# Kernel tuning notes

Measured on AMD Instinct MI355X. Metric: run time of the kernel, lower is better.

Reference implementation:

```python
import jax, jax.numpy as jnp
import numpy as np

B, L, D_IN, D_OUT = 8, 2048, 256, 256


def setup_inputs() -> dict:
    key = jax.random.key(0)
    ks = jax.random.split(key, 7)
    s_in = 1.0 / np.sqrt(D_IN)
    return {
        "x": jax.random.normal(ks[0], (B, L, D_IN), dtype=jnp.float32),
        "Wq": jax.random.uniform(ks[1], (D_OUT, D_IN), jnp.float32, -s_in, s_in),
        "bq": jax.random.uniform(ks[2], (D_OUT,), jnp.float32, -s_in, s_in),
        "Wk": jax.random.uniform(ks[3], (D_OUT, D_IN), jnp.float32, -s_in, s_in),
        "bk": jax.random.uniform(ks[4], (D_OUT,), jnp.float32, -s_in, s_in),
        "Wv": jax.random.uniform(ks[5], (D_OUT, D_IN), jnp.float32, -s_in, s_in),
        "bv": jax.random.uniform(ks[6], (D_OUT,), jnp.float32, -s_in, s_in),
    }


def reference(x, Wq, bq, Wk, bk, Wv, bv):
    # QKV projections (torch Linear: y = x @ W.T + b)
    Q = jnp.einsum("bld,od->blo", x, Wq) + bq  # [B, L, D_OUT]
    K = jnp.einsum("bld,od->blo", x, Wk) + bk
    V = jnp.einsum("bld,od->blo", x, Wv) + bv
    scale = jnp.float32(D_OUT) ** 0.5
    E = jnp.einsum("bqd,bkd->bqk", Q, K) / scale  # [B, L, L]
    # NON-STANDARD: softmax over dim=1 (the query axis / columns of E)
    A = jax.nn.softmax(E, axis=1)
    C = jnp.einsum("bqk,bkd->bqd", A, V)  # [B, L, D_OUT]
    S_p = jnp.concatenate([Q, C], axis=1)  # [B, 2L, D_OUT]
    return (S_p, A)
```

## Files before the change

### kernel.cpp

```cpp
#include <hip/hip_runtime.h>
#include <hip/hip_bf16.h>
#include <stdint.h>

#define B_ 8
#define L_ 2048
#define D_ 256

typedef unsigned short u16;
typedef __attribute__((ext_vector_type(4))) float f32x4;
typedef __attribute__((ext_vector_type(8))) short bf16x8;
typedef __attribute__((ext_vector_type(4))) short s16x4;

__device__ __forceinline__ u16 f2b(float f) {
  union { float f; unsigned u; } v; v.f = f;
  unsigned r = v.u + 0x7FFFu + ((v.u >> 16) & 1u);
  return (u16)(r >> 16);
}

__device__ __forceinline__ float b2f(u16 h) {
  union { unsigned u; float f; } v; v.u = (unsigned)h << 16; return v.f;
}

__device__ __forceinline__ void comb(float& m, float& s, float m2, float s2) {
  float mn = fmaxf(m, m2);
  s = s * __expf(m - mn) + s2 * __expf(m2 - mn);
  m = mn;
}

__device__ __forceinline__ void async_copy16(const void* g, u16* l) {
  __builtin_amdgcn_global_load_lds(
      (const __attribute__((address_space(1))) unsigned*)g,
      (__attribute__((address_space(3))) unsigned*)l,
      16, 0, 0);
}

template<int KD>
__device__ __forceinline__ void gemm_core(const u16* __restrict__ Ag,
                                          const u16* __restrict__ Bg,
                                          int tile_m, int tile_n,
                                          u16* lds_a, u16* lds_b,
                                          f32x4 acc[4][4]) {
  const int tid  = threadIdx.x;
  const int wave = tid >> 6, lane = tid & 63;
  const int qd = lane >> 4, ln = lane & 15;
  const int wm = wave >> 1, wn = wave & 1;
  const int lrow = lane >> 2;
  const int lcol = (lane & 3) * 8;
  const u16* Abase = Ag + (size_t)tile_m * KD + lcol;
  const u16* Bbase = Bg + (size_t)tile_n * KD + lcol;

  for (int k0 = 0; k0 < KD; k0 += 32) {
#pragma unroll
    for (int j = 0; j < 2; ++j) {
      const int r0 = j * 64 + wave * 16;
      async_copy16(Abase + (size_t)(r0 + lrow) * KD + k0, lds_a + r0 * 32);
      async_copy16(Bbase + (size_t)(r0 + lrow) * KD + k0, lds_b + r0 * 32);
    }
    __syncthreads();
    bf16x8 af[4], bg[4];
#pragma unroll
    for (int i = 0; i < 4; ++i) {
      af[i] = *(const bf16x8*)(lds_a + (wm * 64 + i * 16 + ln) * 32 + qd * 8);
      bg[i] = *(const bf16x8*)(lds_b + (wn * 64 + i * 16 + ln) * 32 + qd * 8);
    }
#pragma unroll
    for (int i = 0; i < 4; ++i)
#pragma unroll
      for (int j = 0; j < 4; ++j)
        acc[i][j] = __builtin_amdgcn_mfma_f32_16x16x32_bf16(af[i], bg[j], acc[i][j], 0, 0, 0);
    __syncthreads();
  }
}

__global__ __launch_bounds__(256) void cvt_kernel(const float* __restrict__ x,
    const float* __restrict__ Wq, const float* __restrict__ Wk, const float* __restrict__ Wv,
    u16* __restrict__ xb, u16* __restrict__ Wb) {
  const int i = blockIdx.x * 256 + threadIdx.x;
  const int NX4 = (B_ * L_ * D_) / 4;
  f32x4 v;
  u16* dst;
  if (i < NX4) {
    v = ((const f32x4*)x)[i];
    dst = xb + (size_t)i * 4;
  } else {
    int wi = i - NX4;
    int z = wi >> 14;
    int off = wi & 16383;
    const float* W = (z == 0) ? Wq : (z == 1 ? Wk : Wv);
    v = ((const f32x4*)W)[off];
    dst = Wb + (size_t)z * 65536 + (size_t)off * 4;
  }
  unsigned p0 = (unsigned)f2b(v.x) | ((unsigned)f2b(v.y) << 16);
  unsigned p1 = (unsigned)f2b(v.z) | ((unsigned)f2b(v.w) << 16);
  *(uint2*)dst = make_uint2(p0, p1);
}

__global__ __launch_bounds__(256) void qkv_gemm(const u16* __restrict__ xb, const u16* __restrict__ Wb,
    const float* __restrict__ bq, const float* __restrict__ bk, const float* __restrict__ bv,
    u16* __restrict__ Qb, u16* __restrict__ Kb, u16* __restrict__ Vb,
    float* __restrict__ out_sp) {
  __shared__ u16 lds_a[128 * 32], lds_b[128 * 32];
  const int z = blockIdx.z;
  const float* bias = (z == 0) ? bq : (z == 1 ? bk : bv);
  u16* dst = (z == 0) ? Qb : (z == 1 ? Kb : Vb);
  const int tile_m = blockIdx.x * 128, tile_n = blockIdx.y * 128;
  f32x4 acc[4][4];
#pragma unroll
  for (int i = 0; i < 4; ++i)
#pragma unroll
    for (int j = 0; j < 4; ++j) acc[i][j] = (f32x4){0.f, 0.f, 0.f, 0.f};
  gemm_core<256>(xb, Wb + (size_t)z * 256 * 256, tile_m, tile_n, lds_a, lds_b, acc);

  const int lane = threadIdx.x & 63, wave = threadIdx.x >> 6;
  const int qd = lane >> 4, ln = lane & 15, wm = wave >> 1, wn = wave & 1;
#pragma unroll
  for (int i = 0; i < 4; ++i)
#pragma unroll
    for (int j = 0; j < 4; ++j) {
      const int col = tile_n + wn * 64 + j * 16 + ln;
      const float bvv = bias[col];
      const int row0 = tile_m + wm * 64 + i * 16 + qd * 4;
#pragma unroll
      for (int r = 0; r < 4; ++r) {
        const int row = row0 + r;
        const float val = acc[i][j][r] + bvv;
        dst[(size_t)row * D_ + col] = f2b(val);
        if (z == 0) {
          const int bb = row >> 11, l = row & 2047;
          out_sp[((size_t)bb * (2 * L_) + l) * D_ + col] = val;
        }
      }
    }
}

__global__ __launch_bounds__(256) void transpose_v(const u16* __restrict__ Vb, u16* __restrict__ Vbt) {
  const int b = blockIdx.z;
  const int l0 = blockIdx.x * 64;
  const int d0 = blockIdx.y * 64;
  __shared__ u16 t[64][65];
  const int tx = threadIdx.x & 63;
  const int ty = threadIdx.x >> 6;
  const u16* src = Vb + (size_t)b * L_ * D_;
  for (int j = ty; j < 64; j += 4)
    t[j][tx] = src[(size_t)(l0 + j) * D_ + d0 + tx];
  __syncthreads();
  u16* dst = Vbt + (size_t)b * D_ * L_;
  for (int j = ty; j < 64; j += 4)
    dst[(size_t)(d0 + j) * L_ + l0 + tx] = t[tx][j];
}

__global__ __launch_bounds__(256) void e_gemm(const u16* __restrict__ Qb, const u16* __restrict__ Kb,
                                              u16* __restrict__ Eb16,
                                              float* __restrict__ pm, float* __restrict__ ps) {
  __shared__ u16 lds_a[128 * 32], lds_b[128 * 32];
  __shared__ float sm_m[4][64], sm_s[4][64];
  const int b = blockIdx.z;
  const int tile_m = blockIdx.x * 128, tile_n = blockIdx.y * 128;
  f32x4 acc[4][4];
#pragma unroll
  for (int i = 0; i < 4; ++i)
#pragma unroll
    for (int j = 0; j < 4; ++j) acc[i][j] = (f32x4){0.f, 0.f, 0.f, 0.f};
  gemm_core<256>(Qb + (size_t)b * L_ * D_, Kb + (size_t)b * L_ * D_, tile_m, tile_n, lds_a, lds_b, acc);

  u16* Eb = Eb16 + (size_t)b * L_ * L_;
  const int tid = threadIdx.x;
  const int lane = tid & 63, wave = tid >> 6;
  const int qd = lane >> 4, ln = lane & 15, wm = wave >> 1, wn = wave & 1;
#pragma unroll
  for (int j = 0; j < 4; ++j) {
    const int col = tile_n + wn * 64 + j * 16 + ln;
    const int row0 = tile_m + wm * 64 + qd * 4;
    float m = -1e30f;
#pragma unroll
    for (int i = 0; i < 4; ++i)
#pragma unroll
      for (int r = 0; r < 4; ++r)
        m = fmaxf(m, acc[i][j][r] * 0.0625f);
    float s = 0.f;
#pragma unroll
    for (int i = 0; i < 4; ++i)
#pragma unroll
      for (int r = 0; r < 4; ++r) {
        const float e = acc[i][j][r] * 0.0625f;
        Eb[(size_t)(row0 + i * 16 + r) * L_ + col] = f2b(e);
        s += __expf(e - m);
      }
    comb(m, s, __shfl_xor(m, 16), __shfl_xor(s, 16));
    comb(m, s, __shfl_xor(m, 32), __shfl_xor(s, 32));
    if (qd == 0) { sm_m[wave][j * 16 + ln] = m; sm_s[wave][j * 16 + ln] = s; }
  }
  __syncthreads();
  if (tid < 128) {
    const int w = tid >> 6, c = tid & 63;
    float m = sm_m[w][c], s = sm_s[w][c];
    comb(m, s, sm_m[w + 2][c], sm_s[w + 2][c]);
    const size_t idx = (size_t)blockIdx.x * (B_ * L_) + (size_t)b * L_ + tile_n + w * 64 + c;
    pm[idx] = m;
    ps[idx] = s;
  }
}

__global__ __launch_bounds__(256) void stats_reduce(const float* __restrict__ pm,
                                                    const float* __restrict__ ps,
                                                    float* __restrict__ mOut, float* __restrict__ rOut) {
  const int idx = blockIdx.x * 256 + threadIdx.x;
  float m = -1e30f, s = 0.f;
#pragma unroll
  for (int t = 0; t < 16; ++t)
    comb(m, s, pm[t * (B_ * L_) + idx], ps[t * (B_ * L_) + idx]);
  mOut[idx] = m;
  rOut[idx] = 1.0f / s;
}

__global__ __launch_bounds__(256) void av_fused(const u16* __restrict__ Eb16, const u16* __restrict__ Vbt,
                                                const float* __restrict__ mArr, const float* __restrict__ rArr,
                                                float* __restrict__ Aout, float* __restrict__ out_sp) {
  __shared__ u16 lds_b[256 * 32];
  __shared__ u16 lds_a[32 * 32];
  const int b = blockIdx.y;
  const int tile_m = blockIdx.x * 32;
  const int tid = threadIdx.x;
  const int wave = tid >> 6, lane = tid & 63;
  const int qd = lane >> 4, ln = lane & 15;
  const int lrow = lane >> 2, lcol = (lane & 3) * 8;

  const u16* Vb_ = Vbt + (size_t)b * D_ * L_ + lcol;
  const int arow = tid >> 3, koff = (tid & 7) * 4;
  const u16* Erow = Eb16 + ((size_t)b * L_ + tile_m + arow) * L_ + koff;
  float* Arow = Aout + ((size_t)(b * L_ + tile_m + arow)) * L_ + koff;
  const float* mrow = mArr + (size_t)b * L_ + koff;
  const float* rrow = rArr + (size_t)b * L_ + koff;

  f32x4 acc[2][4];
#pragma unroll
  for (int i = 0; i < 2; ++i)
#pragma unroll
    for (int j = 0; j < 4; ++j) acc[i][j] = (f32x4){0.f, 0.f, 0.f, 0.f};

  for (int k0 = 0; k0 < L_; k0 += 32) {
#pragma unroll
    for (int jj = 0; jj < 4; ++jj) {
      const int r0 = wave * 64 + jj * 16;
      async_copy16(Vb_ + (size_t)(r0 + lrow) * L_ + k0, lds_b + r0 * 32);
    }
    s16x4 ev = *(const s16x4*)(Erow + k0);
    const f32x4 mv = *(const f32x4*)(mrow + k0);
    const f32x4 rv = *(const f32x4*)(rrow + k0);
    f32x4 a;
    a.x = __expf(b2f((u16)ev.x) - mv.x) * rv.x;
    a.y = __expf(b2f((u16)ev.y) - mv.y) * rv.y;
    a.z = __expf(b2f((u16)ev.z) - mv.z) * rv.z;
    a.w = __expf(b2f((u16)ev.w) - mv.w) * rv.w;
    *(f32x4*)(Arow + k0) = a;
    uint2 pk;
    pk.x = (unsigned)f2b(a.x) | ((unsigned)f2b(a.y) << 16);
    pk.y = (unsigned)f2b(a.z) | ((unsigned)f2b(a.w) << 16);
    *(uint2*)(lds_a + (size_t)tid * 4) = pk;
    __syncthreads();

    bf16x8 af[2], bg[4];
#pragma unroll
    for (int i = 0; i < 2; ++i)
      af[i] = *(const bf16x8*)(lds_a + (i * 16 + ln) * 32 + qd * 8);
#pragma unroll
    for (int j = 0; j < 4; ++j)
      bg[j] = *(const bf16x8*)(lds_b + (wave * 64 + j * 16 + ln) * 32 + qd * 8);
#pragma unroll
    for (int i = 0; i < 2; ++i)
#pragma unroll
      for (int j = 0; j < 4; ++j)
        acc[i][j] = __builtin_amdgcn_mfma_f32_16x16x32_bf16(af[i], bg[j], acc[i][j], 0, 0, 0);
    __syncthreads();
  }

#pragma unroll
  for (int i = 0; i < 2; ++i)
#pragma unroll
    for (int j = 0; j < 4; ++j) {
      const int col = wave * 64 + j * 16 + ln;
      const int row0 = tile_m + i * 16 + qd * 4;
#pragma unroll
      for (int r = 0; r < 4; ++r)
        out_sp[((size_t)b * (2 * L_) + L_ + row0 + r) * D_ + col] = acc[i][j][r];
    }
}

extern "C" void kernel_launch(void* const* d_in, const int* in_sizes, int n_in,
                              void* d_out, int out_size, void* d_ws, size_t ws_size,
                              hipStream_t stream) {
  const float* x  = (const float*)d_in[0];
  const float* Wq = (const float*)d_in[1];
  const float* bq = (const float*)d_in[2];
  const float* Wk = (const float*)d_in[3];
  const float* bk = (const float*)d_in[4];
  const float* Wv = (const float*)d_in[5];
  const float* bv = (const float*)d_in[6];

  float* out    = (float*)d_out;
  float* outA   = out + (size_t)B_ * (2 * L_) * D_;

  u16* w    = (u16*)d_ws;
  u16* xb   = w;
  u16* Wb   = xb + 4194304;
  u16* Qb   = Wb + 196608;
  u16* Kb   = Qb + 4194304;
  u16* Vb   = Kb + 4194304;
  u16* Vbt  = Vb + 4194304;
  u16* Eb16 = Vbt + 4194304;
  float* mArr = (float*)(Eb16 + 33554432);
  float* rArr = mArr + B_ * L_;
  float* pm   = rArr + B_ * L_;
  float* ps   = pm + 16 * B_ * L_;

  cvt_kernel<<<4288, 256, 0, stream>>>(x, Wq, Wk, Wv, xb, Wb);
  qkv_gemm<<<dim3(128, 2, 3), 256, 0, stream>>>(xb, Wb, bq, bk, bv, Qb, Kb, Vb, out);
  transpose_v<<<dim3(32, 4, 8), 256, 0, stream>>>(Vb, Vbt);
  e_gemm<<<dim3(16, 16, 8), 256, 0, stream>>>(Qb, Kb, Eb16, pm, ps);
  stats_reduce<<<64, 256, 0, stream>>>(pm, ps, mArr, rArr);
  av_fused<<<dim3(64, 8), 256, 0, stream>>>(Eb16, Vbt, mArr, rArr, outA, out);
}
```

Measured before the change: 319.1 us.

## Stage GEMM epilogues through LDS, fuse V transpose, widen AV k-step

The QKV and E GEMM epilogues now stage their bf16 results in shared memory and write them out as coalesced 16-byte rows instead of scattered 2-byte stores. The V projection writes its transposed layout directly, which removes the separate transpose kernel and its extra round trip through global memory. The av_fused loop now processes 64 columns per step with 8-wide loads and prefetches the next E, m and r values, halving the number of barriers. The cost is more shared-memory use in av_fused and extra barriers in the epilogues.

```diff
diff --git a/kernel.cpp b/kernel.cpp
--- a/kernel.cpp
+++ b/kernel.cpp
@@ -9,7 +9,6 @@
 typedef unsigned short u16;
 typedef __attribute__((ext_vector_type(4))) float f32x4;
 typedef __attribute__((ext_vector_type(8))) short bf16x8;
-typedef __attribute__((ext_vector_type(4))) short s16x4;
 
 __device__ __forceinline__ u16 f2b(float f) {
   union { float f; unsigned u; } v; v.f = f;
@@ -97,62 +96,92 @@
 
 __global__ __launch_bounds__(256) void qkv_gemm(const u16* __restrict__ xb, const u16* __restrict__ Wb,
     const float* __restrict__ bq, const float* __restrict__ bk, const float* __restrict__ bv,
-    u16* __restrict__ Qb, u16* __restrict__ Kb, u16* __restrict__ Vb,
+    u16* __restrict__ Qb, u16* __restrict__ Kb, u16* __restrict__ Vbt,
     float* __restrict__ out_sp) {
-  __shared__ u16 lds_a[128 * 32], lds_b[128 * 32];
+  __shared__ u16 lds[8192];
   const int z = blockIdx.z;
   const float* bias = (z == 0) ? bq : (z == 1 ? bk : bv);
-  u16* dst = (z == 0) ? Qb : (z == 1 ? Kb : Vb);
   const int tile_m = blockIdx.x * 128, tile_n = blockIdx.y * 128;
   f32x4 acc[4][4];
 #pragma unroll
   for (int i = 0; i < 4; ++i)
 #pragma unroll
     for (int j = 0; j < 4; ++j) acc[i][j] = (f32x4){0.f, 0.f, 0.f, 0.f};
-  gemm_core<256>(xb, Wb + (size_t)z * 256 * 256, tile_m, tile_n, lds_a, lds_b, acc);
-
-  const int lane = threadIdx.x & 63, wave = threadIdx.x >> 6;
+  gemm_core<256>(xb, Wb + (size_t)z * 256 * 256, tile_m, tile_n, lds, lds + 4096, acc);
+
+  const int tid = threadIdx.x, lane = tid & 63, wave = tid >> 6;
   const int qd = lane >> 4, ln = lane & 15, wm = wave >> 1, wn = wave & 1;
-#pragma unroll
-  for (int i = 0; i < 4; ++i)
-#pragma unroll
-    for (int j = 0; j < 4; ++j) {
-      const int col = tile_n + wn * 64 + j * 16 + ln;
-      const float bvv = bias[col];
-      const int row0 = tile_m + wm * 64 + i * 16 + qd * 4;
-#pragma unroll
-      for (int r = 0; r < 4; ++r) {
-        const int row = row0 + r;
-        const float val = acc[i][j][r] + bvv;
-        dst[(size_t)row * D_ + col] = f2b(val);
-        if (z == 0) {
-          const int bb = row >> 11, l = row & 2047;
-          out_sp[((size_t)bb * (2 * L_) + l) * D_ + col] = val;
-        }
+
+  if (z < 2) {
+    u16* dst = (z == 0) ? Qb : Kb;
+#pragma unroll
+    for (int p = 0; p < 2; ++p) {
+      __syncthreads();
+      if (wm == p) {
+#pragma unroll
+        for (int i = 0; i < 4; ++i)
+#pragma unroll
+          for (int j = 0; j < 4; ++j) {
+            const int col = wn * 64 + j * 16 + ln;
+            const float bvv = bias[tile_n + col];
+#pragma unroll
+            for (int r = 0; r < 4; ++r) {
+              const int row = i * 16 + qd * 4 + r;
+              const float val = acc[i][j][r] + bvv;
+              lds[row * 128 + col] = f2b(val);
+              if (z == 0) {
+                const int grow = tile_m + p * 64 + row;
+                const int bb = grow >> 11, l = grow & 2047;
+                out_sp[((size_t)bb * (2 * L_) + l) * D_ + tile_n + col] = val;
+              }
+            }
+          }
       }
-    }
-}
-
-__global__ __launch_bounds__(256) void transpose_v(const u16* __restrict__ Vb, u16* __restrict__ Vbt) {
-  const int b = blockIdx.z;
-  const int l0 = blockIdx.x * 64;
-  const int d0 = blockIdx.y * 64;
-  __shared__ u16 t[64][65];
-  const int tx = threadIdx.x & 63;
-  const int ty = threadIdx.x >> 6;
-  const u16* src = Vb + (size_t)b * L_ * D_;
-  for (int j = ty; j < 64; j += 4)
-    t[j][tx] = src[(size_t)(l0 + j) * D_ + d0 + tx];
-  __syncthreads();
-  u16* dst = Vbt + (size_t)b * D_ * L_;
-  for (int j = ty; j < 64; j += 4)
-    dst[(size_t)(d0 + j) * L_ + l0 + tx] = t[tx][j];
+      __syncthreads();
+      const int r = tid >> 2;
+#pragma unroll
+      for (int s = 0; s < 4; ++s) {
+        const int chunk = (tid & 3) + s * 4;
+        bf16x8 v = *(const bf16x8*)(lds + r * 128 + chunk * 8);
+        *(bf16x8*)(dst + (size_t)(tile_m + p * 64 + r) * D_ + tile_n + chunk * 8) = v;
+      }
+    }
+  } else {
+    const int bb = tile_m >> 11, l0 = tile_m & 2047;
+    u16* dstb = Vbt + (size_t)bb * D_ * L_;
+#pragma unroll
+    for (int p = 0; p < 2; ++p) {
+      __syncthreads();
+      if (wn == p) {
+#pragma unroll
+        for (int i = 0; i < 4; ++i)
+#pragma unroll
+          for (int j = 0; j < 4; ++j) {
+            const int col = j * 16 + ln;
+            const float bvv = bias[tile_n + p * 64 + col];
+#pragma unroll
+            for (int r = 0; r < 4; ++r) {
+              const int row = wm * 64 + i * 16 + qd * 4 + r;
+              lds[col * 128 + row] = f2b(acc[i][j][r] + bvv);
+            }
+          }
+      }
+      __syncthreads();
+      const int dr = tid >> 2;
+#pragma unroll
+      for (int s = 0; s < 4; ++s) {
+        const int chunk = (tid & 3) + s * 4;
+        bf16x8 v = *(const bf16x8*)(lds + dr * 128 + chunk * 8);
+        *(bf16x8*)(dstb + (size_t)(tile_n + p * 64 + dr) * L_ + l0 + chunk * 8) = v;
+      }
+    }
+  }
 }
 
 __global__ __launch_bounds__(256) void e_gemm(const u16* __restrict__ Qb, const u16* __restrict__ Kb,
                                               u16* __restrict__ Eb16,
                                               float* __restrict__ pm, float* __restrict__ ps) {
-  __shared__ u16 lds_a[128 * 32], lds_b[128 * 32];
+  __shared__ u16 lds[8192];
   __shared__ float sm_m[4][64], sm_s[4][64];
   const int b = blockIdx.z;
   const int tile_m = blockIdx.x * 128, tile_n = blockIdx.y * 128;
@@ -161,16 +190,15 @@
   for (int i = 0; i < 4; ++i)
 #pragma unroll
     for (int j = 0; j < 4; ++j) acc[i][j] = (f32x4){0.f, 0.f, 0.f, 0.f};
-  gemm_core<256>(Qb + (size_t)b * L_ * D_, Kb + (size_t)b * L_ * D_, tile_m, tile_n, lds_a, lds_b, acc);
+  gemm_core<256>(Qb + (size_t)b * L_ * D_, Kb + (size_t)b * L_ * D_, tile_m, tile_n, lds, lds + 4096, acc);
 
   u16* Eb = Eb16 + (size_t)b * L_ * L_;
   const int tid = threadIdx.x;
   const int lane = tid & 63, wave = tid >> 6;
   const int qd = lane >> 4, ln = lane & 15, wm = wave >> 1, wn = wave & 1;
+
 #pragma unroll
   for (int j = 0; j < 4; ++j) {
-    const int col = tile_n + wn * 64 + j * 16 + ln;
-    const int row0 = tile_m + wm * 64 + qd * 4;
     float m = -1e30f;
 #pragma unroll
     for (int i = 0; i < 4; ++i)
@@ -181,11 +209,8 @@
 #pragma unroll
     for (int i = 0; i < 4; ++i)
 #pragma unroll
-      for (int r = 0; r < 4; ++r) {
-        const float e = acc[i][j][r] * 0.0625f;
-        Eb[(size_t)(row0 + i * 16 + r) * L_ + col] = f2b(e);
-        s += __expf(e - m);
-      }
+      for (int r = 0; r < 4; ++r)
+        s += __expf(acc[i][j][r] * 0.0625f - m);
     comb(m, s, __shfl_xor(m, 16), __shfl_xor(s, 16));
     comb(m, s, __shfl_xor(m, 32), __shfl_xor(s, 32));
     if (qd == 0) { sm_m[wave][j * 16 + ln] = m; sm_s[wave][j * 16 + ln] = s; }
@@ -199,6 +224,32 @@
     pm[idx] = m;
     ps[idx] = s;
   }
+
+#pragma unroll
+  for (int p = 0; p < 2; ++p) {
+    __syncthreads();
+    if (wm == p) {
+#pragma unroll
+      for (int i = 0; i < 4; ++i)
+#pragma unroll
+        for (int j = 0; j < 4; ++j) {
+          const int col = wn * 64 + j * 16 + ln;
+#pragma unroll
+          for (int r = 0; r < 4; ++r) {
+            const int row = i * 16 + qd * 4 + r;
+            lds[row * 128 + col] = f2b(acc[i][j][r] * 0.0625f);
+          }
+        }
+    }
+    __syncthreads();
+    const int r = tid >> 2;
+#pragma unroll
+    for (int s = 0; s < 4; ++s) {
+      const int chunk = (tid & 3) + s * 4;
+      bf16x8 v = *(const bf16x8*)(lds + r * 128 + chunk * 8);
+      *(bf16x8*)(Eb + (size_t)(tile_m + p * 64 + r) * L_ + tile_n + chunk * 8) = v;
+    }
+  }
 }
 
 __global__ __launch_bounds__(256) void stats_reduce(const float* __restrict__ pm,
@@ -216,19 +267,19 @@
 __global__ __launch_bounds__(256) void av_fused(const u16* __restrict__ Eb16, const u16* __restrict__ Vbt,
                                                 const float* __restrict__ mArr, const float* __restrict__ rArr,
                                                 float* __restrict__ Aout, float* __restrict__ out_sp) {
-  __shared__ u16 lds_b[256 * 32];
-  __shared__ u16 lds_a[32 * 32];
+  __shared__ u16 lds_b[256 * 64];
+  __shared__ u16 lds_a[32 * 64];
   const int b = blockIdx.y;
   const int tile_m = blockIdx.x * 32;
   const int tid = threadIdx.x;
   const int wave = tid >> 6, lane = tid & 63;
   const int qd = lane >> 4, ln = lane & 15;
-  const int lrow = lane >> 2, lcol = (lane & 3) * 8;
+  const int lrow = lane >> 3, lcol = (lane & 7) * 8;
 
   const u16* Vb_ = Vbt + (size_t)b * D_ * L_ + lcol;
-  const int arow = tid >> 3, koff = (tid & 7) * 4;
+  const int arow = tid >> 3, koff = (tid & 7) * 8;
   const u16* Erow = Eb16 + ((size_t)b * L_ + tile_m + arow) * L_ + koff;
-  float* Arow = Aout + ((size_t)(b * L_ + tile_m + arow)) * L_ + koff;
+  float* Arow = Aout + ((size_t)b * L_ + tile_m + arow) * L_ + koff;
   const float* mrow = mArr + (size_t)b * L_ + koff;
   const float* rrow = rArr + (size_t)b * L_ + koff;
 
@@ -238,39 +289,55 @@
 #pragma unroll
     for (int j = 0; j < 4; ++j) acc[i][j] = (f32x4){0.f, 0.f, 0.f, 0.f};
 
-  for (int k0 = 0; k0 < L_; k0 += 32) {
-#pragma unroll
-    for (int jj = 0; jj < 4; ++jj) {
-      const int r0 = wave * 64 + jj * 16;
-      async_copy16(Vb_ + (size_t)(r0 + lrow) * L_ + k0, lds_b + r0 * 32);
-    }
-    s16x4 ev = *(const s16x4*)(Erow + k0);
-    const f32x4 mv = *(const f32x4*)(mrow + k0);
-    const f32x4 rv = *(const f32x4*)(rrow + k0);
-    f32x4 a;
-    a.x = __expf(b2f((u16)ev.x) - mv.x) * rv.x;
-    a.y = __expf(b2f((u16)ev.y) - mv.y) * rv.y;
-    a.z = __expf(b2f((u16)ev.z) - mv.z) * rv.z;
-    a.w = __expf(b2f((u16)ev.w) - mv.w) * rv.w;
-    *(f32x4*)(Arow + k0) = a;
-    uint2 pk;
-    pk.x = (unsigned)f2b(a.x) | ((unsigned)f2b(a.y) << 16);
-    pk.y = (unsigned)f2b(a.z) | ((unsigned)f2b(a.w) << 16);
-    *(uint2*)(lds_a + (size_t)tid * 4) = pk;
-    __syncthreads();
-
-    bf16x8 af[2], bg[4];
+  bf16x8 ev = *(const bf16x8*)(Erow);
+  f32x4 mv0 = *(const f32x4*)(mrow),     mv1 = *(const f32x4*)(mrow + 4);
+  f32x4 rv0 = *(const f32x4*)(rrow),     rv1 = *(const f32x4*)(rrow + 4);
+
+  for (int k0 = 0; k0 < L_; k0 += 64) {
+#pragma unroll
+    for (int jj = 0; jj < 8; ++jj) {
+      const int r0 = wave * 64 + jj * 8;
+      async_copy16(Vb_ + (size_t)(r0 + lrow) * L_ + k0, lds_b + r0 * 64);
+    }
+    float a0 = __expf(b2f((u16)ev[0]) - mv0.x) * rv0.x;
+    float a1 = __expf(b2f((u16)ev[1]) - mv0.y) * rv0.y;
+    float a2 = __expf(b2f((u16)ev[2]) - mv0.z) * rv0.z;
+    float a3 = __expf(b2f((u16)ev[3]) - mv0.w) * rv0.w;
+    float a4 = __expf(b2f((u16)ev[4]) - mv1.x) * rv1.x;
+    float a5 = __expf(b2f((u16)ev[5]) - mv1.y) * rv1.y;
+    float a6 = __expf(b2f((u16)ev[6]) - mv1.z) * rv1.z;
+    float a7 = __expf(b2f((u16)ev[7]) - mv1.w) * rv1.w;
+    *(f32x4*)(Arow + k0)     = (f32x4){a0, a1, a2, a3};
+    *(f32x4*)(Arow + k0 + 4) = (f32x4){a4, a5, a6, a7};
+    uint4 pk;
+    pk.x = (unsigned)f2b(a0) | ((unsigned)f2b(a1) << 16);
+    pk.y = (unsigned)f2b(a2) | ((unsigned)f2b(a3) << 16);
+    pk.z = (unsigned)f2b(a4) | ((unsigned)f2b(a5) << 16);
+    pk.w = (unsigned)f2b(a6) | ((unsigned)f2b(a7) << 16);
+    *(uint4*)(lds_a + (size_t)tid * 8) = pk;
+    const int kn = (k0 + 64) & (L_ - 1);
+    ev  = *(const bf16x8*)(Erow + kn);
+    mv0 = *(const f32x4*)(mrow + kn); mv1 = *(const f32x4*)(mrow + kn + 4);
+    rv0 = *(const f32x4*)(rrow + kn); rv1 = *(const f32x4*)(rrow + kn + 4);
+    __syncthreads();
+    bf16x8 af[2][2], bg[4][2];
 #pragma unroll
     for (int i = 0; i < 2; ++i)
-      af[i] = *(const bf16x8*)(lds_a + (i * 16 + ln) * 32 + qd * 8);
+#pragma unroll
+      for (int ks = 0; ks < 2; ++ks)
+        af[i][ks] = *(const bf16x8*)(lds_a + (i * 16 + ln) * 64 + ks * 32 + qd * 8);
 #pragma unroll
     for (int j = 0; j < 4; ++j)
-      bg[j] = *(const bf16x8*)(lds_b + (wave * 64 + j * 16 + ln) * 32 + qd * 8);
-#pragma unroll
-    for (int i = 0; i < 2; ++i)
-#pragma unroll
-      for (int j = 0; j < 4; ++j)
-        acc[i][j] = __builtin_amdgcn_mfma_f32_16x16x32_bf16(af[i], bg[j], acc[i][j], 0, 0, 0);
+#pragma unroll
+      for (int ks = 0; ks < 2; ++ks)
+        bg[j][ks] = *(const bf16x8*)(lds_b + (wave * 64 + j * 16 + ln) * 64 + ks * 32 + qd * 8);
+#pragma unroll
+    for (int ks = 0; ks < 2; ++ks)
+#pragma unroll
+      for (int i = 0; i < 2; ++i)
+#pragma unroll
+        for (int j = 0; j < 4; ++j)
+          acc[i][j] = __builtin_amdgcn_mfma_f32_16x16x32_bf16(af[i][ks], bg[j][ks], acc[i][j], 0, 0, 0);
     __syncthreads();
   }
 
@@ -305,8 +372,7 @@
   u16* Wb   = xb + 4194304;
   u16* Qb   = Wb + 196608;
   u16* Kb   = Qb + 4194304;
-  u16* Vb   = Kb + 4194304;
-  u16* Vbt  = Vb + 4194304;
+  u16* Vbt  = Kb + 4194304;
   u16* Eb16 = Vbt + 4194304;
   float* mArr = (float*)(Eb16 + 33554432);
   float* rArr = mArr + B_ * L_;
@@ -314,8 +380,7 @@
   float* ps   = pm + 16 * B_ * L_;
 
   cvt_kernel<<<4288, 256, 0, stream>>>(x, Wq, Wk, Wv, xb, Wb);
-  qkv_gemm<<<dim3(128, 2, 3), 256, 0, stream>>>(xb, Wb, bq, bk, bv, Qb, Kb, Vb, out);
-  transpose_v<<<dim3(32, 4, 8), 256, 0, stream>>>(Vb, Vbt);
+  qkv_gemm<<<dim3(128, 2, 3), 256, 0, stream>>>(xb, Wb, bq, bk, bv, Qb, Kb, Vbt, out);
   e_gemm<<<dim3(16, 16, 8), 256, 0, stream>>>(Qb, Kb, Eb16, pm, ps);
   stats_reduce<<<64, 256, 0, stream>>>(pm, ps, mArr, rArr);
   av_fused<<<dim3(64, 8), 256, 0, stream>>>(Eb16, Vbt, mArr, rArr, outA, out);
```

Result: faster. 296.8 us (-7.0%).
